# Optimization experiments

Hardware: AMD Instinct MI355X
Metric: run time of the kernel (lower is better)

## Reference

```python
import jax, jax.numpy as jnp
import numpy as np

N_QUBITS = 12
DEPTH = 4
OUT_DIM = 4096
BATCH = 2048
M_IN = 4096


def setup_inputs() -> dict:
    key = jax.random.key(0)
    k1, k2 = jax.random.split(key)
    x = jax.random.normal(k1, (BATCH, M_IN), dtype=jnp.float32)
    w = jax.random.uniform(k2, (DEPTH, N_QUBITS, 3), dtype=jnp.float32) * (2.0 * np.pi)
    return {"x": x, "w": w}


def _rot_matrix(phi, theta, omega):
    # PennyLane Rot(phi, theta, omega) = RZ(omega) @ RY(theta) @ RZ(phi)
    c = jnp.cos(theta / 2)
    s = jnp.sin(theta / 2)
    m = jnp.stack([
        jnp.stack([jnp.exp(-1j * (phi + omega) / 2) * c, -jnp.exp(1j * (phi - omega) / 2) * s]),
        jnp.stack([jnp.exp(-1j * (phi - omega) / 2) * s, jnp.exp(1j * (phi + omega) / 2) * c]),
    ])
    return m.astype(jnp.complex64)


def _apply_1q(s, U, q):
    # s: (B,) + (2,)*n ; wire q lives on axis q+1 (wire 0 = MSB, default.qubit order)
    s = jnp.moveaxis(s, q + 1, -1)
    s = jnp.einsum('...j,ij->...i', s, U)
    return jnp.moveaxis(s, -1, q + 1)


def _cnot(s, c, t):
    # control wire c < target wire t; flip target axis on the control=1 slice
    p0 = s[(slice(None),) * (c + 1) + (0,)]
    p1 = jnp.flip(s[(slice(None),) * (c + 1) + (1,)], axis=t)  # axis t after removing axis c+1
    return jnp.stack([p0, p1], axis=c + 1)


def _layer(s, wl):
    n = N_QUBITS
    for i in range(n):
        s = _apply_1q(s, _rot_matrix(wl[i, 0], wl[i, 1], wl[i, 2]), i)
    for i in range(n):
        for j in range(i + 1, n):
            s = _cnot(s, i, j)
    return s


def reference(x, w):
    B, m = x.shape
    n = N_QUBITS
    # amplitude embedding: per-sample L2 normalize with uniform fallback
    norm = jnp.linalg.norm(x, axis=1, keepdims=True)
    ok = norm > 1e-10
    amp = jnp.where(ok, x / jnp.where(ok, norm, 1.0), 1.0 / np.sqrt(m))
    s = amp.astype(jnp.complex64).reshape((B,) + (2,) * n)
    for layer in range(DEPTH):
        s = _layer(s, w[layer])
    sv = s.reshape(B, -1)
    probs = sv.real ** 2 + sv.imag ** 2
    pn = probs[:, :OUT_DIM]
    tot = jnp.sum(pn, axis=1, keepdims=True)
    okp = tot > 1e-10
    out = jnp.where(okp, pn / jnp.where(okp, tot, 1.0), 1.0 / OUT_DIM)
    return out.astype(x.dtype)
```

## Files before the change

kernel.cpp:

```cpp
#include <hip/hip_runtime.h>
#include <math.h>

#define NQ 12
#define DIM 4096
#define NLAYER 4
#define NT 512

typedef float v2 __attribute__((ext_vector_type(2)));

__device__ __forceinline__ v2 mkv2(float a, float b) { v2 r; r.x = a; r.y = b; return r; }
__device__ __forceinline__ v2 sp(float a) { v2 r; r.x = a; r.y = a; return r; }
__device__ __forceinline__ v2 pkfma(v2 a, float b, v2 c) {
  return __builtin_elementwise_fma(a, sp(b), c);
}

__device__ __forceinline__ int sfun(int z) {
  z ^= z >> 1; z ^= z >> 2; z ^= z >> 4; z ^= z >> 8; return z & (DIM - 1);
}
__device__ __forceinline__ int swz(int s) {
  int m = s ^ ((s >> 6) & 63);
  return m ^ ((m >> 3) & 7);
}

__device__ __forceinline__ v2 block_reduce_sum2(v2 v, v2* red) {
  const int tid = threadIdx.x;
#pragma unroll
  for (int off = 32; off > 0; off >>= 1) {
    v.x += __shfl_down(v.x, off, 64);
    v.y += __shfl_down(v.y, off, 64);
  }
  if ((tid & 63) == 0) red[tid >> 6] = v;
  __syncthreads();
  if (tid == 0) {
    v2 s = sp(0.f);
#pragma unroll
    for (int i = 0; i < NT / 64; ++i) s += red[i];
    red[0] = s;
  }
  __syncthreads();
  v2 r = red[0];
  __syncthreads();
  return r;
}

__device__ __forceinline__ void apply_pair(v2& r0, v2& i0, v2& r1, v2& i1,
    const float2 u00, const float2 u01, const float2 u10, const float2 u11) {
  v2 nr0 = pkfma(i1, -u01.y, pkfma(r1, u01.x, pkfma(i0, -u00.y, r0 * sp(u00.x))));
  v2 ni0 = pkfma(r1,  u01.y, pkfma(i1, u01.x, pkfma(r0,  u00.y, i0 * sp(u00.x))));
  v2 nr1 = pkfma(i1, -u11.y, pkfma(r1, u11.x, pkfma(i0, -u10.y, r0 * sp(u10.x))));
  v2 ni1 = pkfma(r1,  u11.y, pkfma(i1, u11.x, pkfma(r0,  u10.y, i0 * sp(u10.x))));
  r0 = nr0; i0 = ni0; r1 = nr1; i1 = ni1;
}

template <int RT>
__device__ __forceinline__ void gates3(v2 re[8], v2 im[8], const float2* GL) {
#pragma unroll
  for (int i = 0; i < 3; ++i) {
    const int q = 2 + 3 * RT - i;
    const float2 u00 = GL[q * 4 + 0], u01 = GL[q * 4 + 1];
    const float2 u10 = GL[q * 4 + 2], u11 = GL[q * 4 + 3];
#pragma unroll
    for (int pe = 0; pe < 4; ++pe) {
      const int e0 = ((pe >> i) << (i + 1)) | (pe & ((1 << i) - 1));
      const int e1 = e0 | (1 << i);
      apply_pair(re[e0], im[e0], re[e1], im[e1], u00, u01, u10, u11);
    }
  }
}

#define LOAD8(ADDR)                         \
  _Pragma("unroll")                         \
  for (int j = 0; j < 8; ++j) {             \
    const float4 v = st[ADDR[j]];           \
    re[j] = mkv2(v.x, v.y);                 \
    im[j] = mkv2(v.z, v.w);                 \
  }
#define STORE8(ADDR)                        \
  _Pragma("unroll")                         \
  for (int j = 0; j < 8; ++j)               \
    st[ADDR[j]] = make_float4(re[j].x, re[j].y, im[j].x, im[j].y);

__global__ __launch_bounds__(NT, 4) void qsim_kernel(
    const float* __restrict__ x, const float* __restrict__ w,
    float* __restrict__ out) {
  extern __shared__ __align__(16) char smem[];
  float4* st   = (float4*)smem;
  float2* gmat = (float2*)(st + DIM);
  v2*     red  = (v2*)(gmat + NLAYER * NQ * 4);

  const int t = threadIdx.x;
  const int lane = t & 63, wave = t >> 6;
  const int a = t & 7, b = (t >> 3) & 7;
  const long r0 = 2L * blockIdx.x;

  if (t < NLAYER * NQ) {
    const float* wp = w + t * 3;
    float phi = wp[0], th = wp[1], om = wp[2];
    float sn, cc, sa, ca, sb, cb;
    sincosf(0.5f * th, &sn, &cc);
    sincosf(0.5f * (phi + om), &sa, &ca);
    sincosf(0.5f * (phi - om), &sb, &cb);
    float2* g = &gmat[t * 4];
    g[0] = make_float2(ca * cc, -sa * cc);
    g[1] = make_float2(-cb * sn, -sb * sn);
    g[2] = make_float2(cb * sn, -sb * sn);
    g[3] = make_float2(ca * cc, sa * cc);
  }

  const float4* xa = (const float4*)(x + r0 * DIM) + t * 2;
  const float4* xb = (const float4*)(x + (r0 + 1) * DIM) + t * 2;
  const float4 a0 = xa[0], a1 = xa[1], b0 = xb[0], b1 = xb[1];
  const float va[8] = {a0.x, a0.y, a0.z, a0.w, a1.x, a1.y, a1.z, a1.w};
  const float vb[8] = {b0.x, b0.y, b0.z, b0.w, b1.x, b1.y, b1.z, b1.w};
  v2 ss = sp(0.f);
#pragma unroll
  for (int e = 0; e < 8; ++e) { ss.x += va[e] * va[e]; ss.y += vb[e] * vb[e]; }
  const v2 nsq = block_reduce_sum2(ss, red);
  const float n0 = sqrtf(nsq.x), n1 = sqrtf(nsq.y);
  const bool ok0 = n0 > 1e-10f, ok1 = n1 > 1e-10f;
  const float i0f = ok0 ? 1.0f / n0 : 0.f, i1f = ok1 ? 1.0f / n1 : 0.f;
#pragma unroll
  for (int e = 0; e < 8; ++e)
    st[swz(t * 8 + e)] = make_float4(ok0 ? va[e] * i0f : 0.015625f,
                                     ok1 ? vb[e] * i1f : 0.015625f, 0.f, 0.f);

  int p0[8], p1[8], p2[8], p3[8], gd[8];
#pragma unroll
  for (int j = 0; j < 8; ++j) {
    p0[j] = swz(t | (j << 9));
    p1[j] = swz(lane | (j << 6) | (wave << 9));
    p2[j] = swz(a | (j << 3) | (b << 6) | (wave << 9));
    p3[j] = swz(j | (a << 3) | (b << 6) | (wave << 9));
    gd[j] = swz(sfun(t | (j << 9)));
  }
  __syncthreads();

  v2 re[8], im[8];
#pragma unroll
  for (int L = 0; L < NLAYER; ++L) {
    const float2* GL = &gmat[L * NQ * 4];

    if (L == 0) {
      LOAD8(p0)
    } else {
      LOAD8(gd)
    }
    gates3<0>(re, im, GL);
    if (L > 0) __syncthreads();
    STORE8(p0)
    __syncthreads();

    LOAD8(p1)
    gates3<1>(re, im, GL);
    STORE8(p1)
    __syncthreads();

    LOAD8(p2)
    gates3<2>(re, im, GL);
    STORE8(p2)
    __syncthreads();

    LOAD8(p3)
    gates3<3>(re, im, GL);
    STORE8(p3)
    __syncthreads();
  }

  float q0[8], q1[8];
  v2 ps = sp(0.f);
#pragma unroll
  for (int k = 0; k < 8; ++k) {
    const float4 v = st[gd[k]];
    q0[k] = v.x * v.x + v.z * v.z;
    q1[k] = v.y * v.y + v.w * v.w;
    ps.x += q0[k]; ps.y += q1[k];
  }
  const v2 tot = block_reduce_sum2(ps, red);
  const bool k0 = tot.x > 1e-10f, k1 = tot.y > 1e-10f;
  const float t0 = k0 ? 1.0f / tot.x : 0.f, t1 = k1 ? 1.0f / tot.y : 0.f;
  float* o0 = out + r0 * DIM;
  float* o1 = out + (r0 + 1) * DIM;
#pragma unroll
  for (int k = 0; k < 8; ++k) {
    o0[t + k * NT] = k0 ? q0[k] * t0 : (1.0f / DIM);
    o1[t + k * NT] = k1 ? q1[k] * t1 : (1.0f / DIM);
  }
}

extern "C" void kernel_launch(void* const* d_in, const int* in_sizes, int n_in,
                              void* d_out, int out_size, void* d_ws, size_t ws_size,
                              hipStream_t stream) {
  const float* x = (const float*)d_in[0];
  const float* w = (const float*)d_in[1];
  float* out = (float*)d_out;
  const int B = in_sizes[0] / DIM;
  const size_t smem = DIM * sizeof(float4) + NLAYER * NQ * 4 * sizeof(float2)
                    + (NT / 64) * sizeof(v2);
  qsim_kernel<<<B / 2, NT, smem, stream>>>(x, w, out);
}
```

Before: 87.55 us.

## Process four qubits per register pass with 256 threads and XOR address tables

Each thread now holds 16 amplitudes instead of 8 and applies gates to four qubits per pass, so a layer needs three shared-memory passes instead of four. The block shrinks to 256 threads. Per-element swizzled addresses become a base XORed with compile-time tables, which cuts index arithmetic and register use. The cost is higher register pressure and fewer threads per block, which may lower occupancy and latency hiding.

```diff
diff --git a/kernel.cpp b/kernel.cpp
--- a/kernel.cpp
+++ b/kernel.cpp
@@ -4,7 +4,7 @@
 #define NQ 12
 #define DIM 4096
 #define NLAYER 4
-#define NT 512
+#define NT 256
 
 typedef float v2 __attribute__((ext_vector_type(2)));
 
@@ -14,6 +14,13 @@
   return __builtin_elementwise_fma(a, sp(b), c);
 }
 
+constexpr int sfun_c(int z) {
+  z ^= z >> 1; z ^= z >> 2; z ^= z >> 4; z ^= z >> 8; return z & (DIM - 1);
+}
+constexpr int swz_c(int s) {
+  int m = s ^ ((s >> 6) & 63);
+  return m ^ ((m >> 3) & 7);
+}
 __device__ __forceinline__ int sfun(int z) {
   z ^= z >> 1; z ^= z >> 2; z ^= z >> 4; z ^= z >> 8; return z & (DIM - 1);
 }
@@ -21,6 +28,19 @@
   int m = s ^ ((s >> 6) & 63);
   return m ^ ((m >> 3) & 7);
 }
+
+struct KT { int A[16], B[16], C[16], G[16]; };
+constexpr KT mkKT() {
+  KT k{};
+  for (int j = 0; j < 16; ++j) {
+    k.A[j] = swz_c(j << 8);
+    k.B[j] = swz_c(j << 4);
+    k.C[j] = swz_c(j);
+    k.G[j] = swz_c(sfun_c(j << 8));
+  }
+  return k;
+}
+constexpr KT KTab = mkKT();
 
 __device__ __forceinline__ v2 block_reduce_sum2(v2 v, v2* red) {
   const int tid = threadIdx.x;
@@ -52,15 +72,15 @@
   r0 = nr0; i0 = ni0; r1 = nr1; i1 = ni1;
 }
 
-template <int RT>
-__device__ __forceinline__ void gates3(v2 re[8], v2 im[8], const float2* GL) {
-#pragma unroll
-  for (int i = 0; i < 3; ++i) {
-    const int q = 2 + 3 * RT - i;
+template <int QTOP>
+__device__ __forceinline__ void gates4(v2 re[16], v2 im[16], const float2* GL) {
+#pragma unroll
+  for (int i = 0; i < 4; ++i) {
+    const int q = QTOP - i;
     const float2 u00 = GL[q * 4 + 0], u01 = GL[q * 4 + 1];
     const float2 u10 = GL[q * 4 + 2], u11 = GL[q * 4 + 3];
 #pragma unroll
-    for (int pe = 0; pe < 4; ++pe) {
+    for (int pe = 0; pe < 8; ++pe) {
       const int e0 = ((pe >> i) << (i + 1)) | (pe & ((1 << i) - 1));
       const int e1 = e0 | (1 << i);
       apply_pair(re[e0], im[e0], re[e1], im[e1], u00, u01, u10, u11);
@@ -68,19 +88,20 @@
   }
 }
 
-#define LOAD8(ADDR)                         \
-  _Pragma("unroll")                         \
-  for (int j = 0; j < 8; ++j) {             \
-    const float4 v = st[ADDR[j]];           \
-    re[j] = mkv2(v.x, v.y);                 \
-    im[j] = mkv2(v.z, v.w);                 \
-  }
-#define STORE8(ADDR)                        \
-  _Pragma("unroll")                         \
-  for (int j = 0; j < 8; ++j)               \
-    st[ADDR[j]] = make_float4(re[j].x, re[j].y, im[j].x, im[j].y);
-
-__global__ __launch_bounds__(NT, 4) void qsim_kernel(
+#define LOAD16(BASE, KARR)                        \
+  _Pragma("unroll")                               \
+  for (int j = 0; j < 16; ++j) {                  \
+    const float4 v = st[(BASE) ^ KTab.KARR[j]];   \
+    re[j] = mkv2(v.x, v.y);                       \
+    im[j] = mkv2(v.z, v.w);                       \
+  }
+#define STORE16(BASE, KARR)                       \
+  _Pragma("unroll")                               \
+  for (int j = 0; j < 16; ++j)                    \
+    st[(BASE) ^ KTab.KARR[j]] =                   \
+        make_float4(re[j].x, re[j].y, im[j].x, im[j].y);
+
+__global__ __launch_bounds__(NT, 2) void qsim_kernel(
     const float* __restrict__ x, const float* __restrict__ w,
     float* __restrict__ out) {
   extern __shared__ __align__(16) char smem[];
@@ -89,8 +110,7 @@
   v2*     red  = (v2*)(gmat + NLAYER * NQ * 4);
 
   const int t = threadIdx.x;
-  const int lane = t & 63, wave = t >> 6;
-  const int a = t & 7, b = (t >> 3) & 7;
+  const int lane6 = t & 63, w2 = t >> 6;
   const long r0 = 2L * blockIdx.x;
 
   if (t < NLAYER * NQ) {
@@ -107,70 +127,69 @@
     g[3] = make_float2(ca * cc, sa * cc);
   }
 
-  const float4* xa = (const float4*)(x + r0 * DIM) + t * 2;
-  const float4* xb = (const float4*)(x + (r0 + 1) * DIM) + t * 2;
-  const float4 a0 = xa[0], a1 = xa[1], b0 = xb[0], b1 = xb[1];
-  const float va[8] = {a0.x, a0.y, a0.z, a0.w, a1.x, a1.y, a1.z, a1.w};
-  const float vb[8] = {b0.x, b0.y, b0.z, b0.w, b1.x, b1.y, b1.z, b1.w};
+  const float4* xa = (const float4*)(x + r0 * DIM) + t * 4;
+  const float4* xb = (const float4*)(x + (r0 + 1) * DIM) + t * 4;
+  float va[16], vb[16];
+#pragma unroll
+  for (int k = 0; k < 4; ++k) {
+    const float4 A = xa[k], Bv = xb[k];
+    va[k * 4 + 0] = A.x;  va[k * 4 + 1] = A.y;
+    va[k * 4 + 2] = A.z;  va[k * 4 + 3] = A.w;
+    vb[k * 4 + 0] = Bv.x; vb[k * 4 + 1] = Bv.y;
+    vb[k * 4 + 2] = Bv.z; vb[k * 4 + 3] = Bv.w;
+  }
   v2 ss = sp(0.f);
 #pragma unroll
-  for (int e = 0; e < 8; ++e) { ss.x += va[e] * va[e]; ss.y += vb[e] * vb[e]; }
+  for (int e = 0; e < 16; ++e) { ss.x += va[e] * va[e]; ss.y += vb[e] * vb[e]; }
   const v2 nsq = block_reduce_sum2(ss, red);
   const float n0 = sqrtf(nsq.x), n1 = sqrtf(nsq.y);
   const bool ok0 = n0 > 1e-10f, ok1 = n1 > 1e-10f;
   const float i0f = ok0 ? 1.0f / n0 : 0.f, i1f = ok1 ? 1.0f / n1 : 0.f;
-#pragma unroll
-  for (int e = 0; e < 8; ++e)
-    st[swz(t * 8 + e)] = make_float4(ok0 ? va[e] * i0f : 0.015625f,
-                                     ok1 ? vb[e] * i1f : 0.015625f, 0.f, 0.f);
-
-  int p0[8], p1[8], p2[8], p3[8], gd[8];
-#pragma unroll
-  for (int j = 0; j < 8; ++j) {
-    p0[j] = swz(t | (j << 9));
-    p1[j] = swz(lane | (j << 6) | (wave << 9));
-    p2[j] = swz(a | (j << 3) | (b << 6) | (wave << 9));
-    p3[j] = swz(j | (a << 3) | (b << 6) | (wave << 9));
-    gd[j] = swz(sfun(t | (j << 9)));
-  }
-  __syncthreads();
-
-  v2 re[8], im[8];
+
+  const int baseA = swz(t);
+  const int baseB = swz((t & 15) | (w2 << 8) | (((t >> 4) & 3) << 10));
+  const int baseC = swz((lane6 << 4) | (w2 << 10));
+  const int gbase = swz(sfun(t));
+
+#pragma unroll
+  for (int e = 0; e < 16; ++e)
+    st[baseC ^ KTab.C[e]] = make_float4(ok0 ? va[e] * i0f : 0.015625f,
+                                        ok1 ? vb[e] * i1f : 0.015625f, 0.f, 0.f);
+  __syncthreads();
+
+  v2 re[16], im[16];
 #pragma unroll
   for (int L = 0; L < NLAYER; ++L) {
     const float2* GL = &gmat[L * NQ * 4];
 
     if (L == 0) {
-      LOAD8(p0)
+      LOAD16(baseA, A)
+      gates4<3>(re, im, GL);
+      STORE16(baseA, A)
     } else {
-      LOAD8(gd)
+      LOAD16(gbase, G)
+      gates4<3>(re, im, GL);
+      __syncthreads();
+      STORE16(baseA, A)
     }
-    gates3<0>(re, im, GL);
-    if (L > 0) __syncthreads();
-    STORE8(p0)
     __syncthreads();
 
-    LOAD8(p1)
-    gates3<1>(re, im, GL);
-    STORE8(p1)
+    LOAD16(baseB, B)
+    gates4<7>(re, im, GL);
+    STORE16(baseB, B)
     __syncthreads();
 
-    LOAD8(p2)
-    gates3<2>(re, im, GL);
-    STORE8(p2)
+    LOAD16(baseC, C)
+    gates4<11>(re, im, GL);
+    STORE16(baseC, C)
     __syncthreads();
-
-    LOAD8(p3)
-    gates3<3>(re, im, GL);
-    STORE8(p3)
-    __syncthreads();
-  }
-
-  float q0[8], q1[8];
+  }
+
+  float q0[16], q1[16];
   v2 ps = sp(0.f);
 #pragma unroll
-  for (int k = 0; k < 8; ++k) {
-    const float4 v = st[gd[k]];
+  for (int k = 0; k < 16; ++k) {
+    const float4 v = st[gbase ^ KTab.G[k]];
     q0[k] = v.x * v.x + v.z * v.z;
     q1[k] = v.y * v.y + v.w * v.w;
     ps.x += q0[k]; ps.y += q1[k];
@@ -181,7 +200,7 @@
   float* o0 = out + r0 * DIM;
   float* o1 = out + (r0 + 1) * DIM;
 #pragma unroll
-  for (int k = 0; k < 8; ++k) {
+  for (int k = 0; k < 16; ++k) {
     o0[t + k * NT] = k0 ? q0[k] * t0 : (1.0f / DIM);
     o1[t + k * NT] = k1 ? q1[k] * t1 : (1.0f / DIM);
   }
```

New measurement: 87.71 us. About the same (+0.2%).

## Process four samples per block with two shared-memory state buffers

Applied to the files above, without the earlier changes.

Each block now simulates four batch rows instead of two, keeping two interleaved statevector buffers in LDS and applying gate stages to both register sets between each barrier. This halves the number of blocks, shares the gate-matrix setup and the barriers across more work, and gives each thread more independent arithmetic to hide LDS latency. In exchange it doubles LDS per block (about 128KB) and register pressure, and launch bounds drop to one block per CU minimum, so occupancy falls and the grid becomes 512 blocks.

```diff
diff --git a/kernel.cpp b/kernel.cpp
--- a/kernel.cpp
+++ b/kernel.cpp
@@ -22,23 +22,27 @@
   return m ^ ((m >> 3) & 7);
 }
 
-__device__ __forceinline__ v2 block_reduce_sum2(v2 v, v2* red) {
+__device__ __forceinline__ float4 block_reduce_sum4(float4 v, float4* red) {
   const int tid = threadIdx.x;
 #pragma unroll
   for (int off = 32; off > 0; off >>= 1) {
     v.x += __shfl_down(v.x, off, 64);
     v.y += __shfl_down(v.y, off, 64);
+    v.z += __shfl_down(v.z, off, 64);
+    v.w += __shfl_down(v.w, off, 64);
   }
   if ((tid & 63) == 0) red[tid >> 6] = v;
   __syncthreads();
   if (tid == 0) {
-    v2 s = sp(0.f);
-#pragma unroll
-    for (int i = 0; i < NT / 64; ++i) s += red[i];
+    float4 s = make_float4(0.f, 0.f, 0.f, 0.f);
+#pragma unroll
+    for (int i = 0; i < NT / 64; ++i) {
+      s.x += red[i].x; s.y += red[i].y; s.z += red[i].z; s.w += red[i].w;
+    }
     red[0] = s;
   }
   __syncthreads();
-  v2 r = red[0];
+  float4 r = red[0];
   __syncthreads();
   return r;
 }
@@ -68,30 +72,31 @@
   }
 }
 
-#define LOAD8(ADDR)                         \
+#define LOAD8(BUF, RE, IM, ADDR)            \
   _Pragma("unroll")                         \
   for (int j = 0; j < 8; ++j) {             \
-    const float4 v = st[ADDR[j]];           \
-    re[j] = mkv2(v.x, v.y);                 \
-    im[j] = mkv2(v.z, v.w);                 \
-  }
-#define STORE8(ADDR)                        \
+    const float4 v = BUF[ADDR[j]];          \
+    RE[j] = mkv2(v.x, v.y);                 \
+    IM[j] = mkv2(v.z, v.w);                 \
+  }
+#define STORE8(BUF, RE, IM, ADDR)           \
   _Pragma("unroll")                         \
   for (int j = 0; j < 8; ++j)               \
-    st[ADDR[j]] = make_float4(re[j].x, re[j].y, im[j].x, im[j].y);
-
-__global__ __launch_bounds__(NT, 4) void qsim_kernel(
+    BUF[ADDR[j]] = make_float4(RE[j].x, RE[j].y, IM[j].x, IM[j].y);
+
+__global__ __launch_bounds__(NT, 1) void qsim_kernel(
     const float* __restrict__ x, const float* __restrict__ w,
     float* __restrict__ out) {
   extern __shared__ __align__(16) char smem[];
-  float4* st   = (float4*)smem;
-  float2* gmat = (float2*)(st + DIM);
-  v2*     red  = (v2*)(gmat + NLAYER * NQ * 4);
+  float4* stX  = (float4*)smem;
+  float4* stY  = stX + DIM;
+  float2* gmat = (float2*)(stY + DIM);
+  float4* red  = (float4*)(gmat + NLAYER * NQ * 4);
 
   const int t = threadIdx.x;
   const int lane = t & 63, wave = t >> 6;
   const int a = t & 7, b = (t >> 3) & 7;
-  const long r0 = 2L * blockIdx.x;
+  const long r0 = 4L * blockIdx.x;
 
   if (t < NLAYER * NQ) {
     const float* wp = w + t * 3;
@@ -107,22 +112,38 @@
     g[3] = make_float2(ca * cc, sa * cc);
   }
 
-  const float4* xa = (const float4*)(x + r0 * DIM) + t * 2;
-  const float4* xb = (const float4*)(x + (r0 + 1) * DIM) + t * 2;
-  const float4 a0 = xa[0], a1 = xa[1], b0 = xb[0], b1 = xb[1];
-  const float va[8] = {a0.x, a0.y, a0.z, a0.w, a1.x, a1.y, a1.z, a1.w};
-  const float vb[8] = {b0.x, b0.y, b0.z, b0.w, b1.x, b1.y, b1.z, b1.w};
-  v2 ss = sp(0.f);
-#pragma unroll
-  for (int e = 0; e < 8; ++e) { ss.x += va[e] * va[e]; ss.y += vb[e] * vb[e]; }
-  const v2 nsq = block_reduce_sum2(ss, red);
-  const float n0 = sqrtf(nsq.x), n1 = sqrtf(nsq.y);
-  const bool ok0 = n0 > 1e-10f, ok1 = n1 > 1e-10f;
-  const float i0f = ok0 ? 1.0f / n0 : 0.f, i1f = ok1 ? 1.0f / n1 : 0.f;
-#pragma unroll
-  for (int e = 0; e < 8; ++e)
-    st[swz(t * 8 + e)] = make_float4(ok0 ? va[e] * i0f : 0.015625f,
-                                     ok1 ? vb[e] * i1f : 0.015625f, 0.f, 0.f);
+  const float4* xA = (const float4*)(x + (r0 + 0) * DIM) + t * 2;
+  const float4* xB = (const float4*)(x + (r0 + 1) * DIM) + t * 2;
+  const float4* xC = (const float4*)(x + (r0 + 2) * DIM) + t * 2;
+  const float4* xD = (const float4*)(x + (r0 + 3) * DIM) + t * 2;
+  const float4 A0 = xA[0], A1 = xA[1], B0 = xB[0], B1 = xB[1];
+  const float4 C0 = xC[0], C1 = xC[1], D0 = xD[0], D1 = xD[1];
+  const float va[8] = {A0.x, A0.y, A0.z, A0.w, A1.x, A1.y, A1.z, A1.w};
+  const float vb[8] = {B0.x, B0.y, B0.z, B0.w, B1.x, B1.y, B1.z, B1.w};
+  const float vc[8] = {C0.x, C0.y, C0.z, C0.w, C1.x, C1.y, C1.z, C1.w};
+  const float vd[8] = {D0.x, D0.y, D0.z, D0.w, D1.x, D1.y, D1.z, D1.w};
+  float4 ss = make_float4(0.f, 0.f, 0.f, 0.f);
+#pragma unroll
+  for (int e = 0; e < 8; ++e) {
+    ss.x += va[e] * va[e]; ss.y += vb[e] * vb[e];
+    ss.z += vc[e] * vc[e]; ss.w += vd[e] * vd[e];
+  }
+  const float4 nsq = block_reduce_sum4(ss, red);
+  const float nA = sqrtf(nsq.x), nB = sqrtf(nsq.y);
+  const float nC = sqrtf(nsq.z), nD = sqrtf(nsq.w);
+  const bool okA = nA > 1e-10f, okB = nB > 1e-10f;
+  const bool okC = nC > 1e-10f, okD = nD > 1e-10f;
+  const float iA = okA ? 1.0f / nA : 0.f, iB = okB ? 1.0f / nB : 0.f;
+  const float iC = okC ? 1.0f / nC : 0.f, iD = okD ? 1.0f / nD : 0.f;
+
+#pragma unroll
+  for (int e = 0; e < 8; ++e) {
+    const int idx = swz(t * 8 + e);
+    stX[idx] = make_float4(okA ? va[e] * iA : 0.015625f,
+                           okB ? vb[e] * iB : 0.015625f, 0.f, 0.f);
+    stY[idx] = make_float4(okC ? vc[e] * iC : 0.015625f,
+                           okD ? vd[e] * iD : 0.015625f, 0.f, 0.f);
+  }
 
   int p0[8], p1[8], p2[8], p3[8], gd[8];
 #pragma unroll
@@ -135,55 +156,81 @@
   }
   __syncthreads();
 
-  v2 re[8], im[8];
+  v2 xr[8], xi[8], yr[8], yi[8];
 #pragma unroll
   for (int L = 0; L < NLAYER; ++L) {
     const float2* GL = &gmat[L * NQ * 4];
 
     if (L == 0) {
-      LOAD8(p0)
+      LOAD8(stX, xr, xi, p0)
+      LOAD8(stY, yr, yi, p0)
+      gates3<0>(xr, xi, GL);
+      STORE8(stX, xr, xi, p0)
+      gates3<0>(yr, yi, GL);
+      STORE8(stY, yr, yi, p0)
     } else {
-      LOAD8(gd)
+      LOAD8(stX, xr, xi, gd)
+      LOAD8(stY, yr, yi, gd)
+      gates3<0>(xr, xi, GL);
+      gates3<0>(yr, yi, GL);
+      __syncthreads();
+      STORE8(stX, xr, xi, p0)
+      STORE8(stY, yr, yi, p0)
     }
-    gates3<0>(re, im, GL);
-    if (L > 0) __syncthreads();
-    STORE8(p0)
-    __syncthreads();
-
-    LOAD8(p1)
-    gates3<1>(re, im, GL);
-    STORE8(p1)
-    __syncthreads();
-
-    LOAD8(p2)
-    gates3<2>(re, im, GL);
-    STORE8(p2)
-    __syncthreads();
-
-    LOAD8(p3)
-    gates3<3>(re, im, GL);
-    STORE8(p3)
-    __syncthreads();
-  }
-
-  float q0[8], q1[8];
-  v2 ps = sp(0.f);
+    __syncthreads();
+
+    LOAD8(stX, xr, xi, p1)
+    LOAD8(stY, yr, yi, p1)
+    gates3<1>(xr, xi, GL);
+    STORE8(stX, xr, xi, p1)
+    gates3<1>(yr, yi, GL);
+    STORE8(stY, yr, yi, p1)
+    __syncthreads();
+
+    LOAD8(stX, xr, xi, p2)
+    LOAD8(stY, yr, yi, p2)
+    gates3<2>(xr, xi, GL);
+    STORE8(stX, xr, xi, p2)
+    gates3<2>(yr, yi, GL);
+    STORE8(stY, yr, yi, p2)
+    __syncthreads();
+
+    LOAD8(stX, xr, xi, p3)
+    LOAD8(stY, yr, yi, p3)
+    gates3<3>(xr, xi, GL);
+    STORE8(stX, xr, xi, p3)
+    gates3<3>(yr, yi, GL);
+    STORE8(stY, yr, yi, p3)
+    __syncthreads();
+  }
+
+  float qa[8], qb[8], qc[8], qd[8];
+  float4 ps = make_float4(0.f, 0.f, 0.f, 0.f);
 #pragma unroll
   for (int k = 0; k < 8; ++k) {
-    const float4 v = st[gd[k]];
-    q0[k] = v.x * v.x + v.z * v.z;
-    q1[k] = v.y * v.y + v.w * v.w;
-    ps.x += q0[k]; ps.y += q1[k];
-  }
-  const v2 tot = block_reduce_sum2(ps, red);
-  const bool k0 = tot.x > 1e-10f, k1 = tot.y > 1e-10f;
-  const float t0 = k0 ? 1.0f / tot.x : 0.f, t1 = k1 ? 1.0f / tot.y : 0.f;
-  float* o0 = out + r0 * DIM;
-  float* o1 = out + (r0 + 1) * DIM;
+    const float4 vX = stX[gd[k]];
+    const float4 vY = stY[gd[k]];
+    qa[k] = vX.x * vX.x + vX.z * vX.z;
+    qb[k] = vX.y * vX.y + vX.w * vX.w;
+    qc[k] = vY.x * vY.x + vY.z * vY.z;
+    qd[k] = vY.y * vY.y + vY.w * vY.w;
+    ps.x += qa[k]; ps.y += qb[k]; ps.z += qc[k]; ps.w += qd[k];
+  }
+  const float4 tot = block_reduce_sum4(ps, red);
+  const bool kA = tot.x > 1e-10f, kB = tot.y > 1e-10f;
+  const bool kC = tot.z > 1e-10f, kD = tot.w > 1e-10f;
+  const float tA = kA ? 1.0f / tot.x : 0.f, tB = kB ? 1.0f / tot.y : 0.f;
+  const float tC = kC ? 1.0f / tot.z : 0.f, tD = kD ? 1.0f / tot.w : 0.f;
+  float* oA = out + (r0 + 0) * DIM;
+  float* oB = out + (r0 + 1) * DIM;
+  float* oC = out + (r0 + 2) * DIM;
+  float* oD = out + (r0 + 3) * DIM;
 #pragma unroll
   for (int k = 0; k < 8; ++k) {
-    o0[t + k * NT] = k0 ? q0[k] * t0 : (1.0f / DIM);
-    o1[t + k * NT] = k1 ? q1[k] * t1 : (1.0f / DIM);
+    oA[t + k * NT] = kA ? qa[k] * tA : (1.0f / DIM);
+    oB[t + k * NT] = kB ? qb[k] * tB : (1.0f / DIM);
+    oC[t + k * NT] = kC ? qc[k] * tC : (1.0f / DIM);
+    oD[t + k * NT] = kD ? qd[k] * tD : (1.0f / DIM);
   }
 }
 
@@ -194,7 +241,7 @@
   const float* w = (const float*)d_in[1];
   float* out = (float*)d_out;
   const int B = in_sizes[0] / DIM;
-  const size_t smem = DIM * sizeof(float4) + NLAYER * NQ * 4 * sizeof(float2)
-                    + (NT / 64) * sizeof(v2);
-  qsim_kernel<<<B / 2, NT, smem, stream>>>(x, w, out);
-}
+  const size_t smem = 2 * DIM * sizeof(float4) + NLAYER * NQ * 4 * sizeof(float2)
+                    + (NT / 64) * sizeof(float4);
+  qsim_kernel<<<B / 4, NT, smem, stream>>>(x, w, out);
+}
```

Result: slower. 100.9 us (+15.2%).

## Remap state indices so three gate stages stay wave-local and drop barriers

Applied to the files above, without the earlier changes.

Each wave now owns a fixed low-3-bit slice of the 4096-amplitude state, so the first three gate stages of each layer only reshuffle data inside a wave. The two __syncthreads between those stages become compiler memory fences, and only the stage that mixes the low bits keeps a block barrier. Per-thread address arrays are replaced by one base offset per stage XORed with compile-time constant tables, and the LDS swizzle is redesigned to fit the new layout. This cuts barrier stalls and register pressure, but it relies on in-order LDS access within a wave for correctness and may change bank-conflict behaviour.

```diff
diff --git a/kernel.cpp b/kernel.cpp
--- a/kernel.cpp
+++ b/kernel.cpp
@@ -14,13 +14,30 @@
   return __builtin_elementwise_fma(a, sp(b), c);
 }
 
-__device__ __forceinline__ int sfun(int z) {
-  z ^= z >> 1; z ^= z >> 2; z ^= z >> 4; z ^= z >> 8; return z & (DIM - 1);
-}
-__device__ __forceinline__ int swz(int s) {
-  int m = s ^ ((s >> 6) & 63);
-  return m ^ ((m >> 3) & 7);
-}
+#define CFENCE asm volatile("" ::: "memory")
+
+constexpr int sfun_c(int z) { z ^= z >> 1; z ^= z >> 2; z ^= z >> 4; z ^= z >> 8; return z & (DIM - 1); }
+__device__ __forceinline__ int sfun_d(int z) { z ^= z >> 1; z ^= z >> 2; z ^= z >> 4; z ^= z >> 8; return z & (DIM - 1); }
+constexpr int swz_c(int z) {
+  return z ^ ((z >> 6) & 7) ^ ((z >> 9) & 7) ^ (((z >> 9) & 7) << 3);
+}
+__device__ __forceinline__ int swz_d(int z) {
+  return z ^ ((z >> 6) & 7) ^ ((z >> 9) & 7) ^ (((z >> 9) & 7) << 3);
+}
+
+struct KT { int A[8], B[8], C[8], D[8], G[8]; };
+constexpr KT mkKT() {
+  KT k{};
+  for (int j = 0; j < 8; ++j) {
+    k.A[j] = swz_c(j << 9) << 4;
+    k.B[j] = swz_c(j << 6) << 4;
+    k.C[j] = swz_c(j << 3) << 4;
+    k.D[j] = swz_c(j) << 4;
+    k.G[j] = swz_c(sfun_c(j << 9)) << 4;
+  }
+  return k;
+}
+constexpr KT KTab = mkKT();
 
 __device__ __forceinline__ v2 block_reduce_sum2(v2 v, v2* red) {
   const int tid = threadIdx.x;
@@ -68,29 +85,29 @@
   }
 }
 
-#define LOAD8(ADDR)                         \
-  _Pragma("unroll")                         \
-  for (int j = 0; j < 8; ++j) {             \
-    const float4 v = st[ADDR[j]];           \
-    re[j] = mkv2(v.x, v.y);                 \
-    im[j] = mkv2(v.z, v.w);                 \
-  }
-#define STORE8(ADDR)                        \
-  _Pragma("unroll")                         \
-  for (int j = 0; j < 8; ++j)               \
-    st[ADDR[j]] = make_float4(re[j].x, re[j].y, im[j].x, im[j].y);
+#define LOAD8(BB, KARR)                                                \
+  _Pragma("unroll")                                                    \
+  for (int j = 0; j < 8; ++j) {                                        \
+    const float4 v = *(const float4*)(st + ((BB) ^ KTab.KARR[j]));     \
+    re[j] = mkv2(v.x, v.y);                                            \
+    im[j] = mkv2(v.z, v.w);                                            \
+  }
+#define STORE8(BB, KARR)                                               \
+  _Pragma("unroll")                                                    \
+  for (int j = 0; j < 8; ++j)                                          \
+    *(float4*)(st + ((BB) ^ KTab.KARR[j])) =                           \
+        make_float4(re[j].x, re[j].y, im[j].x, im[j].y);
 
 __global__ __launch_bounds__(NT, 4) void qsim_kernel(
     const float* __restrict__ x, const float* __restrict__ w,
     float* __restrict__ out) {
   extern __shared__ __align__(16) char smem[];
-  float4* st   = (float4*)smem;
-  float2* gmat = (float2*)(st + DIM);
+  char*   st   = smem;
+  float2* gmat = (float2*)(smem + DIM * 16);
   v2*     red  = (v2*)(gmat + NLAYER * NQ * 4);
 
   const int t = threadIdx.x;
   const int lane = t & 63, wave = t >> 6;
-  const int a = t & 7, b = (t >> 3) & 7;
   const long r0 = 2L * blockIdx.x;
 
   if (t < NLAYER * NQ) {
@@ -119,20 +136,19 @@
   const float n0 = sqrtf(nsq.x), n1 = sqrtf(nsq.y);
   const bool ok0 = n0 > 1e-10f, ok1 = n1 > 1e-10f;
   const float i0f = ok0 ? 1.0f / n0 : 0.f, i1f = ok1 ? 1.0f / n1 : 0.f;
+
+  const int baseAb = swz_d(wave | (lane << 3)) << 4;
+  const int baseBb = swz_d(wave | ((lane & 7) << 3) | ((lane >> 3) << 9)) << 4;
+  const int baseCb = swz_d(wave | (lane << 6)) << 4;
+  const int baseDb = swz_d((lane << 3) | (wave << 9)) << 4;
+  const int baseGb = swz_d(sfun_d(wave | (lane << 3))) << 4;
+  const int baseOb = swz_d(sfun_d(t)) << 4;
+
 #pragma unroll
   for (int e = 0; e < 8; ++e)
-    st[swz(t * 8 + e)] = make_float4(ok0 ? va[e] * i0f : 0.015625f,
-                                     ok1 ? vb[e] * i1f : 0.015625f, 0.f, 0.f);
-
-  int p0[8], p1[8], p2[8], p3[8], gd[8];
-#pragma unroll
-  for (int j = 0; j < 8; ++j) {
-    p0[j] = swz(t | (j << 9));
-    p1[j] = swz(lane | (j << 6) | (wave << 9));
-    p2[j] = swz(a | (j << 3) | (b << 6) | (wave << 9));
-    p3[j] = swz(j | (a << 3) | (b << 6) | (wave << 9));
-    gd[j] = swz(sfun(t | (j << 9)));
-  }
+    *(float4*)(st + (baseDb ^ KTab.D[e])) =
+        make_float4(ok0 ? va[e] * i0f : 0.015625f,
+                    ok1 ? vb[e] * i1f : 0.015625f, 0.f, 0.f);
   __syncthreads();
 
   v2 re[8], im[8];
@@ -141,28 +157,27 @@
     const float2* GL = &gmat[L * NQ * 4];
 
     if (L == 0) {
-      LOAD8(p0)
+      LOAD8(baseAb, A)
+      gates3<0>(re, im, GL);
+      STORE8(baseAb, A)
     } else {
-      LOAD8(gd)
+      LOAD8(baseGb, G)
+      gates3<0>(re, im, GL);
+      __syncthreads();
+      STORE8(baseAb, A)
     }
-    gates3<0>(re, im, GL);
-    if (L > 0) __syncthreads();
-    STORE8(p0)
+    CFENCE;
+    LOAD8(baseBb, B)
+    gates3<1>(re, im, GL);
+    STORE8(baseBb, B)
+    CFENCE;
+    LOAD8(baseCb, C)
+    gates3<2>(re, im, GL);
+    STORE8(baseCb, C)
     __syncthreads();
-
-    LOAD8(p1)
-    gates3<1>(re, im, GL);
-    STORE8(p1)
-    __syncthreads();
-
-    LOAD8(p2)
-    gates3<2>(re, im, GL);
-    STORE8(p2)
-    __syncthreads();
-
-    LOAD8(p3)
+    LOAD8(baseDb, D)
     gates3<3>(re, im, GL);
-    STORE8(p3)
+    STORE8(baseDb, D)
     __syncthreads();
   }
 
@@ -170,7 +185,7 @@
   v2 ps = sp(0.f);
 #pragma unroll
   for (int k = 0; k < 8; ++k) {
-    const float4 v = st[gd[k]];
+    const float4 v = *(const float4*)(st + (baseOb ^ KTab.G[k]));
     q0[k] = v.x * v.x + v.z * v.z;
     q1[k] = v.y * v.y + v.w * v.w;
     ps.x += q0[k]; ps.y += q1[k];
@@ -194,7 +209,7 @@
   const float* w = (const float*)d_in[1];
   float* out = (float*)d_out;
   const int B = in_sizes[0] / DIM;
-  const size_t smem = DIM * sizeof(float4) + NLAYER * NQ * 4 * sizeof(float2)
+  const size_t smem = DIM * 16 + NLAYER * NQ * 4 * sizeof(float2)
                     + (NT / 64) * sizeof(v2);
   qsim_kernel<<<B / 2, NT, smem, stream>>>(x, w, out);
 }
```

New measurement: 147.6 us. +68.6%, slower.
